# Kernel tuning notes

Hardware: AMD Instinct MI355X
Metric: run time of the kernel (lower is better)

## Reference

```python
import jax, jax.numpy as jnp
import numpy as np

N_POINTS = 262144
NUM_ENC = 6      # F
NUM_FEATS = 16   # C
LOG2_RES = 5
STD = 0.2


def setup_inputs() -> dict:
    key = jax.random.key(0)
    k1, k2 = jax.random.split(key)
    points = jax.random.normal(k1, (N_POINTS, 3), dtype=jnp.float32)
    # freqs = 2 ** linspace(0, F-1, F) = [1,2,4,8,16,32]
    freqs = 2.0 ** jnp.linspace(0.0, NUM_ENC - 1.0, NUM_ENC).astype(jnp.float32)
    res = 2 ** LOG2_RES
    features = jax.random.normal(k2, (NUM_ENC * 2 * 3, NUM_FEATS, res, 1), dtype=jnp.float32) * STD
    return {"points": points, "freqs": freqs, "features": features}


def _forward(points, freqs, features):
    n = points.shape[0]
    F = freqs.shape[0]
    C = features.shape[1]
    res = features.shape[2]
    # --- pos_encode ---
    fp = points[:, None, :] * freqs[None, :, None]          # (n, F, 3)
    enc = jnp.stack((jnp.sin(fp), jnp.cos(fp)), axis=-2)    # (n, F, 2, 3)
    encs = enc.reshape(n, F * 2 * 3).T                       # (G=F*2*3, n), values in [-1,1]
    # --- encoder: grid_sample(features, grid=[x=0, y=encs], align_corners=True) ---
    # features: (G, C, H=res, W=1); x=0 with W=1 -> column 0; bilinear only along H.
    g = jnp.transpose(features[..., 0], (0, 2, 1))           # (G, res, C)
    iy = (encs + 1.0) * 0.5 * (res - 1)                      # (G, n), align_corners=True mapping
    iy0 = jnp.floor(iy)
    w1 = iy - iy0                                            # weight for upper neighbor
    i0 = jnp.clip(iy0.astype(jnp.int32), 0, res - 1)
    i1 = jnp.clip(i0 + 1, 0, res - 1)                        # clamp safe: w1==0 at boundary
    take = jax.vmap(lambda tbl, idx: tbl[idx])               # per-grid gather
    v0 = take(g, i0)                                         # (G, n, C)
    v1 = take(g, i1)                                         # (G, n, C)
    fs = v0 * (1.0 - w1)[..., None] + v1 * w1[..., None]     # (G, n, C)
    fs = jnp.swapaxes(fs, 1, 2)                              # (G, C, n), matches torch (G,C,1,N)
    # raw contiguous reinterpretation (36 -> F,3,2) exactly as torch .view does
    fs = fs.reshape(F, 3, 2, C, n) + encs.reshape(F, 3, 2, 1, n)
    return jnp.transpose(fs, (4, 3, 0, 1, 2)).reshape(n, -1)  # (n, C*F*3*2)


def reference(points, freqs, features):
    return _forward(points, freqs, features)
```

## Files before the change

### kernel.cpp

```cpp
#include <hip/hip_runtime.h>

#define NPTS   262144
#define NG     36
#define NC     16
#define RES    32
#define NROWS  (NG * NC)
#define PADR   33
#define TABF   (NROWS * PADR)

#define K1_BLOCK 256
#define K2_BLOCK 1024
#define K2_GRID  512
#define TOTAL_Q  (NPTS * 144)
#define K2_ITERS (TOTAL_Q / (K2_BLOCK * K2_GRID))

__global__ __launch_bounds__(K1_BLOCK) void encode_kernel(
    const float* __restrict__ points, float* __restrict__ sval)
{
    const int p = blockIdx.x * K1_BLOCK + threadIdx.x;
    const float x = points[p * 3 + 0];
    const float y = points[p * 3 + 1];
    const float z = points[p * 3 + 2];
    float v[NG];
    #pragma unroll
    for (int f = 0; f < 6; ++f) {
        const float w = (float)(1 << f) * 0.15915494309189535f;
        #pragma unroll
        for (int d = 0; d < 3; ++d) {
            const float coord = (d == 0) ? x : ((d == 1) ? y : z);
            const float r = __builtin_amdgcn_fractf(coord * w);
            v[f * 6 + d]     = __builtin_amdgcn_sinf(r);
            v[f * 6 + 3 + d] = __builtin_amdgcn_cosf(r);
        }
    }
    float4* __restrict__ dst = (float4*)(sval + (size_t)p * NG);
    #pragma unroll
    for (int j = 0; j < 9; ++j) dst[j] = ((const float4*)v)[j];
}

__global__ __launch_bounds__(K2_BLOCK, 8) void gather_kernel(
    const float* __restrict__ features,
    const float* __restrict__ sval,
    float* __restrict__ out)
{
    __shared__ float tab[TABF];
    for (int idx = threadIdx.x; idx < TABF; idx += K2_BLOCK) {
        const int row = idx / PADR;
        const int col = idx - row * PADR;
        tab[idx] = (col < RES) ? features[row * RES + col] : 0.f;
    }
    __syncthreads();

    const unsigned tid = blockIdx.x * K2_BLOCK + threadIdx.x;
    const unsigned T   = K2_BLOCK * K2_GRID;
    float4* __restrict__ out4 = (float4*)out;

    #pragma unroll 2
    for (int it = 0; it < K2_ITERS; ++it) {
        const unsigned q    = tid + (unsigned)it * T;
        const unsigned phat = q / 144u;
        const unsigned rq   = q - phat * 144u;
        const unsigned c    = rq / 9u;
        const unsigned m    = rq - c * 9u;
        const float4 v4 = *(const float4*)&sval[phat * 36u + m * 4u];
        const int base  = (int)((m * 4u * NC + c) * PADR);

        float res[4];
        const float vv[4] = { v4.x, v4.y, v4.z, v4.w };
        #pragma unroll
        for (int k = 0; k < 4; ++k) {
            const float val = vv[k];
            const float iy  = __builtin_fmaf(val, 15.5f, 15.5f);
            int i0 = (int)iy;
            i0 = i0 < 0 ? 0 : (i0 > RES - 1 ? RES - 1 : i0);
            const float w = iy - (float)i0;
            const float* __restrict__ row = &tab[base + k * (NC * PADR) + i0];
            const float v0 = row[0];
            const float v1 = row[1];
            res[k] = __builtin_fmaf(w, v1 - v0, v0) + val;
        }
        out4[q] = make_float4(res[0], res[1], res[2], res[3]);
    }
}

extern "C" void kernel_launch(void* const* d_in, const int* in_sizes, int n_in,
                              void* d_out, int out_size, void* d_ws, size_t ws_size,
                              hipStream_t stream) {
    const float* points   = (const float*)d_in[0];
    const float* features = (const float*)d_in[2];
    float* out  = (float*)d_out;
    float* sval = (float*)d_ws;

    encode_kernel<<<dim3(NPTS / K1_BLOCK), dim3(K1_BLOCK), 0, stream>>>(points, sval);
    gather_kernel<<<dim3(K2_GRID), dim3(K2_BLOCK), 0, stream>>>(features, sval, out);
}
```

Before: 656.1 us.

## Use 576-thread blocks with loop-invariant per-thread indexing and nontemporal stores

```diff
diff --git a/kernel.cpp b/kernel.cpp
--- a/kernel.cpp
+++ b/kernel.cpp
@@ -9,10 +9,12 @@
 #define TABF   (NROWS * PADR)
 
 #define K1_BLOCK 256
-#define K2_BLOCK 1024
+#define K2_BLOCK 576
 #define K2_GRID  512
-#define TOTAL_Q  (NPTS * 144)
-#define K2_ITERS (TOTAL_Q / (K2_BLOCK * K2_GRID))
+#define PTS_PER_BLOCK 512
+#define K2_ITERS 128
+
+typedef float v4f __attribute__((ext_vector_type(4)));
 
 __global__ __launch_bounds__(K1_BLOCK) void encode_kernel(
     const float* __restrict__ points, float* __restrict__ sval)
@@ -33,12 +35,12 @@
             v[f * 6 + 3 + d] = __builtin_amdgcn_cosf(r);
         }
     }
-    float4* __restrict__ dst = (float4*)(sval + (size_t)p * NG);
+    v4f* __restrict__ dst = (v4f*)(sval + (size_t)p * NG);
     #pragma unroll
-    for (int j = 0; j < 9; ++j) dst[j] = ((const float4*)v)[j];
+    for (int j = 0; j < 9; ++j) dst[j] = ((const v4f*)v)[j];
 }
 
-__global__ __launch_bounds__(K2_BLOCK, 8) void gather_kernel(
+__global__ __launch_bounds__(K2_BLOCK, 5) void gather_kernel(
     const float* __restrict__ features,
     const float* __restrict__ sval,
     float* __restrict__ out)
@@ -51,35 +53,32 @@
     }
     __syncthreads();
 
-    const unsigned tid = blockIdx.x * K2_BLOCK + threadIdx.x;
-    const unsigned T   = K2_BLOCK * K2_GRID;
-    float4* __restrict__ out4 = (float4*)out;
+    const int tid = threadIdx.x;
+    const int rq  = tid % 144;
+    const int c   = rq / 9;
+    const int m   = rq - c * 9;
+    const int tb0 = (m * 4 * NC + c) * PADR;
+
+    const int phat0 = blockIdx.x * PTS_PER_BLOCK + tid / 144;
+    const v4f* __restrict__ sv = (const v4f*)sval + (size_t)phat0 * 9 + m;
+    v4f* __restrict__ o = (v4f*)out + (size_t)blockIdx.x * (PTS_PER_BLOCK * 144) + tid;
 
     #pragma unroll 2
     for (int it = 0; it < K2_ITERS; ++it) {
-        const unsigned q    = tid + (unsigned)it * T;
-        const unsigned phat = q / 144u;
-        const unsigned rq   = q - phat * 144u;
-        const unsigned c    = rq / 9u;
-        const unsigned m    = rq - c * 9u;
-        const float4 v4 = *(const float4*)&sval[phat * 36u + m * 4u];
-        const int base  = (int)((m * 4u * NC + c) * PADR);
-
-        float res[4];
-        const float vv[4] = { v4.x, v4.y, v4.z, v4.w };
+        const v4f v4 = sv[it * 36];
+        v4f res;
         #pragma unroll
         for (int k = 0; k < 4; ++k) {
-            const float val = vv[k];
+            const float val = v4[k];
             const float iy  = __builtin_fmaf(val, 15.5f, 15.5f);
-            int i0 = (int)iy;
-            i0 = i0 < 0 ? 0 : (i0 > RES - 1 ? RES - 1 : i0);
-            const float w = iy - (float)i0;
-            const float* __restrict__ row = &tab[base + k * (NC * PADR) + i0];
+            const int   i0  = (int)iy;
+            const float w   = iy - (float)i0;
+            const float* __restrict__ row = &tab[tb0 + k * (NC * PADR) + i0];
             const float v0 = row[0];
             const float v1 = row[1];
             res[k] = __builtin_fmaf(w, v1 - v0, v0) + val;
         }
-        out4[q] = make_float4(res[0], res[1], res[2], res[3]);
+        __builtin_nontemporal_store(res, &o[it * K2_BLOCK]);
     }
 }
 
```

After: 624.2 us. -4.9%, faster.
